# Kernel optimization log

Measured on AMD Instinct MI355X. Metric: run time of the kernel, lower is better.

## Reference

```python
import jax, jax.numpy as jnp
import numpy as np

N_NODES = 50000
N_EDGES = 800000
IN_DIM, HID_DIM, OUT_DIM = 128, 64, 64


def spmm(row, col, val, dense):
    # sparse [N,N] (COO) @ dense [N,D] -> [N,D]
    gathered = dense[col] * val[:, None]          # [E, D]
    return jax.ops.segment_sum(gathered, row, num_segments=N_NODES)


def setup_inputs() -> dict:
    key = jax.random.key(0)
    ks = jax.random.split(key, 8)
    stdv1 = 1.0 / np.sqrt(HID_DIM)
    stdv2 = 1.0 / np.sqrt(OUT_DIM)
    return {
        "x": jax.random.normal(ks[0], (N_NODES, IN_DIM), dtype=jnp.float32),
        "edge_row": jax.random.randint(ks[1], (N_EDGES,), 0, N_NODES, dtype=jnp.int32),
        "edge_col": jax.random.randint(ks[2], (N_EDGES,), 0, N_NODES, dtype=jnp.int32),
        "edge_val": jax.random.uniform(ks[3], (N_EDGES,), dtype=jnp.float32),
        "W1": jax.random.uniform(ks[4], (IN_DIM, HID_DIM), jnp.float32, -stdv1, stdv1),
        "b1": jax.random.uniform(ks[5], (HID_DIM,), jnp.float32, -stdv1, stdv1),
        "W2": jax.random.uniform(ks[6], (HID_DIM, OUT_DIM), jnp.float32, -stdv2, stdv2),
        "b2": jax.random.uniform(ks[7], (OUT_DIM,), jnp.float32, -stdv2, stdv2),
    }


def reference(x, edge_row, edge_col, edge_val, W1, b1, W2, b2):
    # layer 1: support = x @ W1; out = adj @ support + b1; relu
    h = jax.nn.relu(spmm(edge_row, edge_col, edge_val, x @ W1) + b1)
    # dropout: eval mode (training=False) -> identity
    # layer 2
    return spmm(edge_row, edge_col, edge_val, h @ W2) + b2
```

## Files before the change

### kernel.cpp

```cpp
#include <hip/hip_runtime.h>


#define N_NODES 50000
#define N_EDGES 800000
#define IN_DIM  128
#define HID_DIM 64
#define OUT_DIM 64

#define RB   256
#define NB   ((N_NODES + RB - 1) / RB)
#define EPB  4096
#define NBLK_E ((N_EDGES + EPB - 1) / EPB)
#define BCAP 5120
#define GEMM1_GRID ((N_NODES + 31) / 32)

typedef __attribute__((ext_vector_type(8))) short bf16x8;
typedef __attribute__((ext_vector_type(4))) float f32x4;

__device__ inline unsigned short f2bf(float x) {
    unsigned u = __float_as_uint(x);
    return (unsigned short)((u + 0x7FFFu + ((u >> 16) & 1u)) >> 16);
}
__device__ inline float bf2f(unsigned v) {
    return __uint_as_float(v << 16);
}

__global__ __launch_bounds__(256) void k_prep(
    const float* __restrict__ W1, unsigned short* __restrict__ Wt1,
    const float* __restrict__ W2, unsigned short* __restrict__ Wt2,
    int* __restrict__ bcur)
{
    int b = blockIdx.x, t = threadIdx.x;
    if (b < 32) {
        int e = b * 256 + t;
        int c = e / IN_DIM, k = e % IN_DIM;
        Wt1[c * IN_DIM + k] = f2bf(W1[k * HID_DIM + c]);
    } else if (b < 48) {
        int e2 = (b - 32) * 256 + t;
        int c = e2 / HID_DIM, k = e2 % HID_DIM;
        Wt2[c * HID_DIM + k] = f2bf(W2[k * OUT_DIM + c]);
    } else {
        if (t < NB) bcur[t] = 0;
    }
}

template <int K, bool IN_BF16>
__device__ __forceinline__ void gemm_body(
    unsigned short* __restrict__ Al, unsigned short* __restrict__ Bl,
    const void* __restrict__ Xv, const unsigned short* __restrict__ Wt,
    unsigned short* __restrict__ out, int bid, int t)
{
    int m0 = bid * 32;
    #pragma unroll
    for (int i = 0; i < K / 32; ++i) {
        int u4 = i * 256 + t;
        int col = (u4 * 8) / K, k = (u4 * 8) % K;
        uint4 w = ((const uint4*)Wt)[u4];
        int byte = (col * K + k) * 2;
        byte ^= ((col & 7) << 4);
        *(uint4*)((char*)Bl + byte) = w;
    }
    if (IN_BF16) {
        const unsigned short* X = (const unsigned short*)Xv;
        int row = t / (K / 8), k = (t % (K / 8)) * 8;
        int grow = m0 + row;
        uint4 v = make_uint4(0, 0, 0, 0);
        if (grow < N_NODES)
            v = *(const uint4*)(X + (size_t)grow * K + k);
        int byte = (row * K + k) * 2;
        byte ^= ((row & 7) << 4);
        *(uint4*)((char*)Al + byte) = v;
    } else {
        const float* X = (const float*)Xv;
        #pragma unroll
        for (int i = 0; i < K / 64; ++i) {
            int f8 = i * 256 + t;
            int row = (f8 * 8) / K, k = (f8 * 8) % K;
            int grow = m0 + row;
            float4 xa = make_float4(0.f, 0.f, 0.f, 0.f), xb = xa;
            if (grow < N_NODES) {
                const float4* src = (const float4*)(X + (size_t)grow * K + k);
                xa = src[0];
                xb = src[1];
            }
            uint4 v;
            v.x = (unsigned)f2bf(xa.x) | ((unsigned)f2bf(xa.y) << 16);
            v.y = (unsigned)f2bf(xa.z) | ((unsigned)f2bf(xa.w) << 16);
            v.z = (unsigned)f2bf(xb.x) | ((unsigned)f2bf(xb.y) << 16);
            v.w = (unsigned)f2bf(xb.z) | ((unsigned)f2bf(xb.w) << 16);
            int byte = (row * K + k) * 2;
            byte ^= ((row & 7) << 4);
            *(uint4*)((char*)Al + byte) = v;
        }
    }
    __syncthreads();

    int w = t >> 6, l = t & 63;
    int lr0 = (w & 1) * 16;
    int c0  = (w >> 1) * 32;
    int lrow = lr0 + (l & 15);
    int kb = (l >> 4) * 8;
    int col0 = c0 + (l & 15), col1 = col0 + 16;
    f32x4 acc0 = {0.f, 0.f, 0.f, 0.f}, acc1 = {0.f, 0.f, 0.f, 0.f};
    #pragma unroll
    for (int kc = 0; kc < K / 32; ++kc) {
        int ka = kc * 32 + kb;
        int ab = (lrow * K + ka) * 2;  ab ^= ((lrow & 7) << 4);
        int bb0 = (col0 * K + ka) * 2; bb0 ^= ((col0 & 7) << 4);
        int bb1 = (col1 * K + ka) * 2; bb1 ^= ((col1 & 7) << 4);
        bf16x8 a  = *(const bf16x8*)((const char*)Al + ab);
        bf16x8 b0 = *(const bf16x8*)((const char*)Bl + bb0);
        bf16x8 b1 = *(const bf16x8*)((const char*)Bl + bb1);
        acc0 = __builtin_amdgcn_mfma_f32_16x16x32_bf16(a, b0, acc0, 0, 0, 0);
        acc1 = __builtin_amdgcn_mfma_f32_16x16x32_bf16(a, b1, acc1, 0, 0, 0);
    }
    int grow0 = m0 + lr0 + (l >> 4) * 4;
    #pragma unroll
    for (int j = 0; j < 4; ++j) {
        int gr = grow0 + j;
        if (gr < N_NODES) {
            out[(size_t)gr * 64 + col0] = f2bf(acc0[j]);
            out[(size_t)gr * 64 + col1] = f2bf(acc1[j]);
        }
    }
}

__global__ __launch_bounds__(256) void k_mega1(
    const float* __restrict__ X, const unsigned short* __restrict__ Wt1,
    unsigned short* __restrict__ support,
    const int* __restrict__ erow, const int* __restrict__ ecol,
    const float* __restrict__ eval_, int* __restrict__ bcur,
    uint2* __restrict__ bucketed)
{
    __shared__ __align__(16) unsigned char smem[35392];
    int t = threadIdx.x;
    if (blockIdx.x < GEMM1_GRID) {
        gemm_body<IN_DIM, false>((unsigned short*)smem,
                                 (unsigned short*)(smem + 8192),
                                 X, Wt1, support, blockIdx.x, t);
        return;
    }
    uint2* sbuf  = (uint2*)smem;
    int*   lc    = (int*)(smem + 32768);
    int*   scr   = (int*)(smem + 33568);
    int*   lbase = (int*)(smem + 34592);
    int blk = blockIdx.x - GEMM1_GRID;
    if (t < NB) lc[t] = 0;
    __syncthreads();
    int base = blk * EPB;
    int ne_total = min(EPB, N_EDGES - base);
    int bkt[16], rnk[16];
    unsigned w0v[16], vv[16];
    #pragma unroll 4
    for (int i = 0; i < 16; ++i) {
        int e = base + i * 256 + t;
        bkt[i] = -1;
        if (e < N_EDGES) {
            unsigned r = (unsigned)erow[e];
            bkt[i] = (int)(r >> 8);
            w0v[i] = (unsigned)ecol[e] | ((r & 255u) << 16)
                     | ((unsigned)(r >> 8) << 24);
            vv[i] = __float_as_uint(eval_[e]);
            rnk[i] = atomicAdd(&lc[bkt[i]], 1);
        }
    }
    __syncthreads();
    int cnt = (t < NB) ? lc[t] : 0;
    scr[t] = cnt;
    __syncthreads();
    #pragma unroll
    for (int off = 1; off < 256; off <<= 1) {
        int add = (t >= off) ? scr[t - off] : 0;
        __syncthreads();
        scr[t] += add;
        __syncthreads();
    }
    int excl = scr[t] - cnt;
    __syncthreads();
    scr[t] = excl;
    if (t < NB) lbase[t] = cnt ? atomicAdd(&bcur[t], cnt) : 0;
    __syncthreads();
    #pragma unroll 4
    for (int i = 0; i < 16; ++i)
        if (bkt[i] >= 0)
            sbuf[scr[bkt[i]] + rnk[i]] = make_uint2(w0v[i], vv[i]);
    __syncthreads();
    #pragma unroll 4
    for (int i = 0; i < 16; ++i) {
        int idx = i * 256 + t;
        if (idx < ne_total) {
            uint2 p = sbuf[idx];
            int bk = (int)(p.x >> 24);
            bucketed[(size_t)bk * BCAP + lbase[bk] + (idx - scr[bk])] = p;
        }
    }
}

__global__ __launch_bounds__(256) void k_bfinal(
    const int* __restrict__ bcur, const uint2* __restrict__ bucketed,
    uint2* __restrict__ pairs, int2* __restrict__ offs2)
{
    __shared__ uint2 ebuf[BCAP];
    __shared__ int rcnt[256];
    __shared__ int rsc[256];
    int t = threadIdx.x, b = blockIdx.x;
    int ne = bcur[b];
    int base0 = b * BCAP;
    rcnt[t] = 0;
    __syncthreads();
    for (int i = t; i < ne; i += 256) {
        uint2 p = bucketed[(size_t)base0 + i];
        ebuf[i] = p;
        atomicAdd(&rcnt[(p.x >> 16) & 255], 1);
    }
    __syncthreads();
    int v = rcnt[t];
    rsc[t] = v;
    __syncthreads();
    #pragma unroll
    for (int off = 1; off < 256; off <<= 1) {
        int add = (t >= off) ? rsc[t - off] : 0;
        __syncthreads();
        rsc[t] += add;
        __syncthreads();
    }
    int start = base0 + rsc[t] - v;
    int gr = (b << 8) + t;
    if (gr < N_NODES) offs2[gr] = make_int2(start, start + v);
    rcnt[t] = start;
    __syncthreads();
    for (int i = t; i < ne; i += 256) {
        uint2 p = ebuf[i];
        int pos = atomicAdd(&rcnt[(p.x >> 16) & 255], 1);
        pairs[pos] = make_uint2(p.x & 0xFFFFu, p.y);
    }
}

template <bool APPLY_RELU, bool OUT_BF16>
__global__ __launch_bounds__(256) void k_gather(
    const int2* __restrict__ offs2, const uint2* __restrict__ pairs,
    const unsigned short* __restrict__ dense, const float* __restrict__ bias,
    void* __restrict__ outp)
{
    int t = threadIdx.x;
    int r = __builtin_amdgcn_readfirstlane(blockIdx.x * 4 + (t >> 6));
    int d = t & 63;
    int2 oe = offs2[r];
    int e0 = oe.x, e1 = oe.y;
    float a[8];
    a[0] = bias[d];
    #pragma unroll
    for (int i = 1; i < 8; ++i) a[i] = 0.f;
    int e = e0;
    for (; e + 8 <= e1; e += 8) {
        uint2 p[8];
        #pragma unroll
        for (int i = 0; i < 8; ++i) p[i] = pairs[e + i];
        unsigned v[8];
        #pragma unroll
        for (int i = 0; i < 8; ++i) v[i] = dense[(size_t)p[i].x * 64u + d];
        #pragma unroll
        for (int i = 0; i < 8; ++i)
            a[i] = fmaf(__uint_as_float(p[i].y), bf2f(v[i]), a[i]);
    }
    if (e + 4 <= e1) {
        uint2 p[4];
        #pragma unroll
        for (int i = 0; i < 4; ++i) p[i] = pairs[e + i];
        unsigned v[4];
        #pragma unroll
        for (int i = 0; i < 4; ++i) v[i] = dense[(size_t)p[i].x * 64u + d];
        #pragma unroll
        for (int i = 0; i < 4; ++i)
            a[i] = fmaf(__uint_as_float(p[i].y), bf2f(v[i]), a[i]);
        e += 4;
    }
    for (; e < e1; ++e) {
        uint2 p = pairs[e];
        a[0] = fmaf(__uint_as_float(p.y),
                    bf2f(dense[(size_t)p.x * 64u + d]), a[0]);
    }
    float acc = ((a[0] + a[1]) + (a[2] + a[3])) +
                ((a[4] + a[5]) + (a[6] + a[7]));
    if (APPLY_RELU) acc = fmaxf(acc, 0.f);
    if (OUT_BF16)
        ((unsigned short*)outp)[(size_t)r * 64 + d] = f2bf(acc);
    else
        ((float*)outp)[(size_t)r * 64 + d] = acc;
}

__global__ __launch_bounds__(256) void k_gemm2(
    const unsigned short* __restrict__ X, const unsigned short* __restrict__ Wt,
    unsigned short* __restrict__ out)
{
    __shared__ unsigned short Al[32 * HID_DIM];
    __shared__ unsigned short Bl[64 * HID_DIM];
    gemm_body<HID_DIM, true>(Al, Bl, X, Wt, out, blockIdx.x, threadIdx.x);
}

extern "C" void kernel_launch(void* const* d_in, const int* in_sizes, int n_in,
                              void* d_out, int out_size, void* d_ws, size_t ws_size,
                              hipStream_t stream)
{
    const float* x     = (const float*)d_in[0];
    const int*   erow  = (const int*)d_in[1];
    const int*   ecol  = (const int*)d_in[2];
    const float* eval_ = (const float*)d_in[3];
    const float* W1    = (const float*)d_in[4];
    const float* b1    = (const float*)d_in[5];
    const float* W2    = (const float*)d_in[6];
    const float* b2    = (const float*)d_in[7];
    float* out = (float*)d_out;

    uint2* pairs    = (uint2*)d_ws;
    uint2* bucketed = pairs + (size_t)NB * BCAP;
    unsigned short* support = (unsigned short*)(bucketed + (size_t)NB * BCAP);
    unsigned short* agg1 = support + (size_t)N_NODES * 64;
    unsigned short* Wt1 = agg1 + (size_t)N_NODES * 64;
    unsigned short* Wt2 = Wt1 + IN_DIM * HID_DIM;
    int*  bcur  = (int*)(Wt2 + HID_DIM * OUT_DIM);
    int2* offs2 = (int2*)(bcur + NB);

    const int row_grid = N_NODES / 4;

    k_prep<<<49, 256, 0, stream>>>(W1, Wt1, W2, Wt2, bcur);
    k_mega1<<<GEMM1_GRID + NBLK_E, 256, 0, stream>>>(
        x, Wt1, support, erow, ecol, eval_, bcur, bucketed);
    k_bfinal<<<NB, 256, 0, stream>>>(bcur, bucketed, pairs, offs2);
    k_gather<true, true><<<row_grid, 256, 0, stream>>>(
        offs2, pairs, support, b1, agg1);
    k_gemm2<<<GEMM1_GRID, 256, 0, stream>>>(agg1, Wt2, support);
    k_gather<false, false><<<row_grid, 256, 0, stream>>>(
        offs2, pairs, support, b2, out);
}
```

Before: 96.24 us.

## Fuse bucket finalization with first SpMM and halve row-bucket size

The bucket-finalize pass and the layer-1 gather are merged into one kernel, k_spmm1, with 512 threads per block. It sorts each bucket's edges into row order in shared memory and aggregates directly from shared column/value arrays, removing a launch and a global re-read of the sorted pairs. Row buckets shrink from 256 to 128 rows, so k_mega1 now needs a two-part scan because there are more than 256 buckets. The layer-2 gather now handles 8 rows per wave. The trade-off is far fewer blocks and waves, so latency hiding for the random support gathers may get worse.

New measurement: 122.0 us. +26.7%, slower.

```diff
diff --git a/kernel.cpp b/kernel.cpp
--- a/kernel.cpp
+++ b/kernel.cpp
@@ -7,11 +7,11 @@
 #define HID_DIM 64
 #define OUT_DIM 64
 
-#define RB   256
-#define NB   ((N_NODES + RB - 1) / RB)
+#define RB   128
+#define NBK  ((N_NODES + RB - 1) / RB)
 #define EPB  4096
 #define NBLK_E ((N_EDGES + EPB - 1) / EPB)
-#define BCAP 5120
+#define BCAP 2560
 #define GEMM1_GRID ((N_NODES + 31) / 32)
 
 typedef __attribute__((ext_vector_type(8))) short bf16x8;
@@ -40,7 +40,7 @@
         int c = e2 / HID_DIM, k = e2 % HID_DIM;
         Wt2[c * HID_DIM + k] = f2bf(W2[k * OUT_DIM + c]);
     } else {
-        if (t < NB) bcur[t] = 0;
+        for (int i = t; i < NBK; i += 256) bcur[i] = 0;
     }
 }
 
@@ -132,7 +132,7 @@
     const float* __restrict__ eval_, int* __restrict__ bcur,
     uint2* __restrict__ bucketed)
 {
-    __shared__ __align__(16) unsigned char smem[35392];
+    __shared__ __align__(16) unsigned char smem[38080];
     int t = threadIdx.x;
     if (blockIdx.x < GEMM1_GRID) {
         gemm_body<IN_DIM, false>((unsigned short*)smem,
@@ -142,10 +142,10 @@
     }
     uint2* sbuf  = (uint2*)smem;
     int*   lc    = (int*)(smem + 32768);
-    int*   scr   = (int*)(smem + 33568);
-    int*   lbase = (int*)(smem + 34592);
+    int*   scr   = (int*)(smem + 34432);
+    int*   lbase = (int*)(smem + 36480);
     int blk = blockIdx.x - GEMM1_GRID;
-    if (t < NB) lc[t] = 0;
+    for (int i = t; i < NBK; i += 256) lc[i] = 0;
     __syncthreads();
     int base = blk * EPB;
     int ne_total = min(EPB, N_EDGES - base);
@@ -157,16 +157,16 @@
         bkt[i] = -1;
         if (e < N_EDGES) {
             unsigned r = (unsigned)erow[e];
-            bkt[i] = (int)(r >> 8);
-            w0v[i] = (unsigned)ecol[e] | ((r & 255u) << 16)
-                     | ((unsigned)(r >> 8) << 24);
+            bkt[i] = (int)(r >> 7);
+            w0v[i] = (unsigned)ecol[e] | ((r & 127u) << 16)
+                     | ((r >> 7) << 23);
             vv[i] = __float_as_uint(eval_[e]);
             rnk[i] = atomicAdd(&lc[bkt[i]], 1);
         }
     }
     __syncthreads();
-    int cnt = (t < NB) ? lc[t] : 0;
-    scr[t] = cnt;
+    int c0 = lc[t], c1 = (t + 256 < NBK) ? lc[t + 256] : 0;
+    scr[t] = c0 + c1;
     __syncthreads();
     #pragma unroll
     for (int off = 1; off < 256; off <<= 1) {
@@ -175,118 +175,184 @@
         scr[t] += add;
         __syncthreads();
     }
-    int excl = scr[t] - cnt;
-    __syncthreads();
-    scr[t] = excl;
-    if (t < NB) lbase[t] = cnt ? atomicAdd(&bcur[t], cnt) : 0;
+    __syncthreads();
+    int pairExcl = scr[t] - (c0 + c1);
+    __shared__ int totFirst;
+    if (t == 255) totFirst = 0;
+    __syncthreads();
+    scr[t] = c0;
+    __syncthreads();
+    #pragma unroll
+    for (int off = 1; off < 256; off <<= 1) {
+        int add = (t >= off) ? scr[t - off] : 0;
+        __syncthreads();
+        scr[t] += add;
+        __syncthreads();
+    }
+    int exclA = scr[t] - c0;
+    int sumA  = scr[255];
+    __syncthreads();
+    scr[t] = c1;
+    __syncthreads();
+    #pragma unroll
+    for (int off = 1; off < 256; off <<= 1) {
+        int add = (t >= off) ? scr[t - off] : 0;
+        __syncthreads();
+        scr[t] += add;
+        __syncthreads();
+    }
+    int exclB = sumA + scr[t] - c1;
+    __syncthreads();
+    scr[t] = exclA;
+    if (t + 256 < NBK) lbase[t + 256] = 0;
+    __syncthreads();
+    if (t + 256 < NBK) scr[t + 256 - 256] = exclA;
+    __shared__ int scrHi[256];
+    scrHi[t] = exclB;
+    if (t < NBK && t < 256)
+        lbase[t] = c0 ? atomicAdd(&bcur[t], c0) : 0;
+    if (t + 256 < NBK)
+        lbase[t + 256] = c1 ? atomicAdd(&bcur[t + 256], c1) : 0;
     __syncthreads();
     #pragma unroll 4
     for (int i = 0; i < 16; ++i)
-        if (bkt[i] >= 0)
-            sbuf[scr[bkt[i]] + rnk[i]] = make_uint2(w0v[i], vv[i]);
+        if (bkt[i] >= 0) {
+            int st = (bkt[i] < 256) ? scr[bkt[i]] : scrHi[bkt[i] - 256];
+            sbuf[st + rnk[i]] = make_uint2(w0v[i], vv[i]);
+        }
     __syncthreads();
     #pragma unroll 4
     for (int i = 0; i < 16; ++i) {
         int idx = i * 256 + t;
         if (idx < ne_total) {
             uint2 p = sbuf[idx];
-            int bk = (int)(p.x >> 24);
-            bucketed[(size_t)bk * BCAP + lbase[bk] + (idx - scr[bk])] = p;
-        }
-    }
-}
-
-__global__ __launch_bounds__(256) void k_bfinal(
+            int bk = (int)(p.x >> 23);
+            int st = (bk < 256) ? scr[bk] : scrHi[bk - 256];
+            bucketed[(size_t)bk * BCAP + lbase[bk] + (idx - st)] = p;
+        }
+    }
+}
+
+__global__ __launch_bounds__(512) void k_spmm1(
     const int* __restrict__ bcur, const uint2* __restrict__ bucketed,
-    uint2* __restrict__ pairs, int2* __restrict__ offs2)
+    const unsigned short* __restrict__ support, const float* __restrict__ b1,
+    uint2* __restrict__ pairs, int2* __restrict__ offs2,
+    unsigned short* __restrict__ agg1)
 {
     __shared__ uint2 ebuf[BCAP];
-    __shared__ int rcnt[256];
-    __shared__ int rsc[256];
+    __shared__ unsigned short scol[BCAP];
+    __shared__ float sval[BCAP];
+    __shared__ int rcnt[RB], lstart[RB], rcur[RB];
     int t = threadIdx.x, b = blockIdx.x;
     int ne = bcur[b];
-    int base0 = b * BCAP;
-    rcnt[t] = 0;
-    __syncthreads();
-    for (int i = t; i < ne; i += 256) {
-        uint2 p = bucketed[(size_t)base0 + i];
+    size_t base0 = (size_t)b * BCAP;
+    if (t < RB) rcnt[t] = 0;
+    __syncthreads();
+    for (int i = t; i < ne; i += 512) {
+        uint2 p = bucketed[base0 + i];
         ebuf[i] = p;
-        atomicAdd(&rcnt[(p.x >> 16) & 255], 1);
-    }
-    __syncthreads();
-    int v = rcnt[t];
-    rsc[t] = v;
-    __syncthreads();
-    #pragma unroll
-    for (int off = 1; off < 256; off <<= 1) {
-        int add = (t >= off) ? rsc[t - off] : 0;
-        __syncthreads();
-        rsc[t] += add;
-        __syncthreads();
-    }
-    int start = base0 + rsc[t] - v;
-    int gr = (b << 8) + t;
-    if (gr < N_NODES) offs2[gr] = make_int2(start, start + v);
-    rcnt[t] = start;
-    __syncthreads();
-    for (int i = t; i < ne; i += 256) {
+        atomicAdd(&rcnt[(p.x >> 16) & 127], 1);
+    }
+    __syncthreads();
+    if (t < 64) {
+        int c0 = rcnt[2 * t], c1 = rcnt[2 * t + 1];
+        int s = c0 + c1, inc = s;
+        #pragma unroll
+        for (int off = 1; off < 64; off <<= 1) {
+            int o = __shfl_up(inc, off, 64);
+            if (t >= off) inc += o;
+        }
+        int excl = inc - s;
+        lstart[2 * t] = excl;
+        lstart[2 * t + 1] = excl + c0;
+        rcur[2 * t] = excl;
+        rcur[2 * t + 1] = excl + c0;
+        int gr = b * RB + 2 * t;
+        int gs = (int)base0 + excl;
+        if (gr < N_NODES) offs2[gr] = make_int2(gs, gs + c0);
+        if (gr + 1 < N_NODES) offs2[gr + 1] = make_int2(gs + c0, gs + c0 + c1);
+    }
+    __syncthreads();
+    for (int i = t; i < ne; i += 512) {
         uint2 p = ebuf[i];
-        int pos = atomicAdd(&rcnt[(p.x >> 16) & 255], 1);
-        pairs[pos] = make_uint2(p.x & 0xFFFFu, p.y);
-    }
-}
-
-template <bool APPLY_RELU, bool OUT_BF16>
-__global__ __launch_bounds__(256) void k_gather(
+        int row = (p.x >> 16) & 127;
+        int pos = atomicAdd(&rcur[row], 1);
+        scol[pos] = (unsigned short)(p.x & 0xFFFFu);
+        sval[pos] = __uint_as_float(p.y);
+        pairs[base0 + pos] = make_uint2(p.x & 0xFFFFu, p.y);
+    }
+    __syncthreads();
+    int w = t >> 6, d = t & 63;
+    #pragma unroll 1
+    for (int j = 0; j < 16; ++j) {
+        int rl = w * 16 + j;
+        int gr = b * RB + rl;
+        if (gr >= N_NODES) continue;
+        int e0 = lstart[rl], e1 = rcur[rl];
+        float a[8];
+        a[0] = b1[d];
+        #pragma unroll
+        for (int i = 1; i < 8; ++i) a[i] = 0.f;
+        int e = e0;
+        for (; e + 8 <= e1; e += 8) {
+            unsigned short c[8];
+            float vv[8];
+            #pragma unroll
+            for (int i = 0; i < 8; ++i) { c[i] = scol[e + i]; vv[i] = sval[e + i]; }
+            unsigned v[8];
+            #pragma unroll
+            for (int i = 0; i < 8; ++i) v[i] = support[(size_t)c[i] * 64u + d];
+            #pragma unroll
+            for (int i = 0; i < 8; ++i) a[i] = fmaf(vv[i], bf2f(v[i]), a[i]);
+        }
+        for (; e < e1; ++e)
+            a[0] = fmaf(sval[e], bf2f(support[(size_t)scol[e] * 64u + d]), a[0]);
+        float acc = ((a[0] + a[1]) + (a[2] + a[3])) +
+                    ((a[4] + a[5]) + (a[6] + a[7]));
+        acc = fmaxf(acc, 0.f);
+        agg1[(size_t)gr * 64 + d] = f2bf(acc);
+    }
+}
+
+__global__ __launch_bounds__(256) void k_gather2(
     const int2* __restrict__ offs2, const uint2* __restrict__ pairs,
     const unsigned short* __restrict__ dense, const float* __restrict__ bias,
-    void* __restrict__ outp)
+    float* __restrict__ outp)
 {
     int t = threadIdx.x;
-    int r = __builtin_amdgcn_readfirstlane(blockIdx.x * 4 + (t >> 6));
-    int d = t & 63;
-    int2 oe = offs2[r];
-    int e0 = oe.x, e1 = oe.y;
-    float a[8];
-    a[0] = bias[d];
-    #pragma unroll
-    for (int i = 1; i < 8; ++i) a[i] = 0.f;
-    int e = e0;
-    for (; e + 8 <= e1; e += 8) {
-        uint2 p[8];
+    int w = t >> 6, d = t & 63;
+    int rbase = __builtin_amdgcn_readfirstlane((blockIdx.x * 4 + w) * 8);
+    #pragma unroll 1
+    for (int j = 0; j < 8; ++j) {
+        int r = rbase + j;
+        if (r >= N_NODES) continue;
+        int2 oe = offs2[r];
+        int e0 = oe.x, e1 = oe.y;
+        float a[8];
+        a[0] = bias[d];
         #pragma unroll
-        for (int i = 0; i < 8; ++i) p[i] = pairs[e + i];
-        unsigned v[8];
-        #pragma unroll
-        for (int i = 0; i < 8; ++i) v[i] = dense[(size_t)p[i].x * 64u + d];
-        #pragma unroll
-        for (int i = 0; i < 8; ++i)
-            a[i] = fmaf(__uint_as_float(p[i].y), bf2f(v[i]), a[i]);
-    }
-    if (e + 4 <= e1) {
-        uint2 p[4];
-        #pragma unroll
-        for (int i = 0; i < 4; ++i) p[i] = pairs[e + i];
-        unsigned v[4];
-        #pragma unroll
-        for (int i = 0; i < 4; ++i) v[i] = dense[(size_t)p[i].x * 64u + d];
-        #pragma unroll
-        for (int i = 0; i < 4; ++i)
-            a[i] = fmaf(__uint_as_float(p[i].y), bf2f(v[i]), a[i]);
-        e += 4;
-    }
-    for (; e < e1; ++e) {
-        uint2 p = pairs[e];
-        a[0] = fmaf(__uint_as_float(p.y),
-                    bf2f(dense[(size_t)p.x * 64u + d]), a[0]);
-    }
-    float acc = ((a[0] + a[1]) + (a[2] + a[3])) +
-                ((a[4] + a[5]) + (a[6] + a[7]));
-    if (APPLY_RELU) acc = fmaxf(acc, 0.f);
-    if (OUT_BF16)
-        ((unsigned short*)outp)[(size_t)r * 64 + d] = f2bf(acc);
-    else
-        ((float*)outp)[(size_t)r * 64 + d] = acc;
+        for (int i = 1; i < 8; ++i) a[i] = 0.f;
+        int e = e0;
+        for (; e + 8 <= e1; e += 8) {
+            uint2 p[8];
+            #pragma unroll
+            for (int i = 0; i < 8; ++i) p[i] = pairs[e + i];
+            unsigned v[8];
+            #pragma unroll
+            for (int i = 0; i < 8; ++i) v[i] = dense[(size_t)p[i].x * 64u + d];
+            #pragma unroll
+            for (int i = 0; i < 8; ++i)
+                a[i] = fmaf(__uint_as_float(p[i].y), bf2f(v[i]), a[i]);
+        }
+        for (; e < e1; ++e) {
+            uint2 p = pairs[e];
+            a[0] = fmaf(__uint_as_float(p.y),
+                        bf2f(dense[(size_t)p.x * 64u + d]), a[0]);
+        }
+        float acc = ((a[0] + a[1]) + (a[2] + a[3])) +
+                    ((a[4] + a[5]) + (a[6] + a[7]));
+        outp[(size_t)r * 64 + d] = acc;
+    }
 }
 
 __global__ __launch_bounds__(256) void k_gemm2(
@@ -313,23 +379,20 @@
     float* out = (float*)d_out;
 
     uint2* pairs    = (uint2*)d_ws;
-    uint2* bucketed = pairs + (size_t)NB * BCAP;
-    unsigned short* support = (unsigned short*)(bucketed + (size_t)NB * BCAP);
+    uint2* bucketed = pairs + (size_t)NBK * BCAP;
+    unsigned short* support = (unsigned short*)(bucketed + (size_t)NBK * BCAP);
     unsigned short* agg1 = support + (size_t)N_NODES * 64;
     unsigned short* Wt1 = agg1 + (size_t)N_NODES * 64;
     unsigned short* Wt2 = Wt1 + IN_DIM * HID_DIM;
     int*  bcur  = (int*)(Wt2 + HID_DIM * OUT_DIM);
-    int2* offs2 = (int2*)(bcur + NB);
-
-    const int row_grid = N_NODES / 4;
+    int2* offs2 = (int2*)(bcur + NBK + 1);
 
     k_prep<<<49, 256, 0, stream>>>(W1, Wt1, W2, Wt2, bcur);
     k_mega1<<<GEMM1_GRID + NBLK_E, 256, 0, stream>>>(
         x, Wt1, support, erow, ecol, eval_, bcur, bucketed);
-    k_bfinal<<<NB, 256, 0, stream>>>(bcur, bucketed, pairs, offs2);
-    k_gather<true, true><<<row_grid, 256, 0, stream>>>(
-        offs2, pairs, support, b1, agg1);
+    k_spmm1<<<NBK, 512, 0, stream>>>(
+        bcur, bucketed, support, b1, pairs, offs2, agg1);
     k_gemm2<<<GEMM1_GRID, 256, 0, stream>>>(agg1, Wt2, support);
-    k_gather<false, false><<<row_grid, 256, 0, stream>>>(
+    k_gather2<<<(N_NODES + 31) / 32, 256, 0, stream>>>(
         offs2, pairs, support, b2, out);
 }
```

## Split fused GEMM1/bucket-scatter kernel into separate launches with smaller edge blocks

Applied to the files above, without the earlier changes.

Replaces the combined kernel that ran the first GEMM and the edge bucket scatter in one grid with separate scatter and GEMM1 kernels. The scatter now handles 1024 edges per block instead of 4096, cutting per-thread register arrays and shared memory so more blocks can be resident. This gives up the concurrency between the GEMM and the scatter, adds a launch, and raises global atomic traffic on the bucket counters.

Measured after the change: 98.86 us. 2.7% more time.

```diff
diff --git a/kernel.cpp b/kernel.cpp
--- a/kernel.cpp
+++ b/kernel.cpp
@@ -9,10 +9,10 @@
 
 #define RB   256
 #define NB   ((N_NODES + RB - 1) / RB)
-#define EPB  4096
+#define EPB  1024
 #define NBLK_E ((N_EDGES + EPB - 1) / EPB)
 #define BCAP 5120
-#define GEMM1_GRID ((N_NODES + 31) / 32)
+#define GEMM_GRID ((N_NODES + 31) / 32)
 
 typedef __attribute__((ext_vector_type(8))) short bf16x8;
 typedef __attribute__((ext_vector_type(4))) float f32x4;
@@ -41,6 +41,106 @@
         Wt2[c * HID_DIM + k] = f2bf(W2[k * OUT_DIM + c]);
     } else {
         if (t < NB) bcur[t] = 0;
+    }
+}
+
+__global__ __launch_bounds__(256) void k_bscatter(
+    const int* __restrict__ erow, const int* __restrict__ ecol,
+    const float* __restrict__ eval_, int* __restrict__ bcur,
+    uint2* __restrict__ bucketed)
+{
+    __shared__ uint2 sbuf[EPB];
+    __shared__ int lc[NB];
+    __shared__ int scr[256];
+    __shared__ int lbase[NB];
+    int t = threadIdx.x;
+    if (t < NB) lc[t] = 0;
+    __syncthreads();
+    int base = blockIdx.x * EPB;
+    int ne = min(EPB, N_EDGES - base);
+    int bkt[4], rnk[4];
+    unsigned w0v[4], vv[4];
+    #pragma unroll
+    for (int i = 0; i < 4; ++i) {
+        int e = base + i * 256 + t;
+        bkt[i] = -1;
+        if (e < N_EDGES) {
+            unsigned r = (unsigned)erow[e];
+            bkt[i] = (int)(r >> 8);
+            w0v[i] = (unsigned)ecol[e] | ((r & 255u) << 16) | ((r >> 8) << 24);
+            vv[i] = __float_as_uint(eval_[e]);
+            rnk[i] = atomicAdd(&lc[bkt[i]], 1);
+        }
+    }
+    __syncthreads();
+    int cnt = (t < NB) ? lc[t] : 0;
+    scr[t] = cnt;
+    __syncthreads();
+    #pragma unroll
+    for (int off = 1; off < 256; off <<= 1) {
+        int add = (t >= off) ? scr[t - off] : 0;
+        __syncthreads();
+        scr[t] += add;
+        __syncthreads();
+    }
+    int excl = scr[t] - cnt;
+    __syncthreads();
+    scr[t] = excl;
+    if (t < NB) lbase[t] = cnt ? atomicAdd(&bcur[t], cnt) : 0;
+    __syncthreads();
+    #pragma unroll
+    for (int i = 0; i < 4; ++i)
+        if (bkt[i] >= 0)
+            sbuf[scr[bkt[i]] + rnk[i]] = make_uint2(w0v[i], vv[i]);
+    __syncthreads();
+    #pragma unroll
+    for (int i = 0; i < 4; ++i) {
+        int idx = i * 256 + t;
+        if (idx < ne) {
+            uint2 p = sbuf[idx];
+            int bk = (int)(p.x >> 24);
+            bucketed[(size_t)bk * BCAP + lbase[bk] + (idx - scr[bk])] = p;
+        }
+    }
+}
+
+__global__ __launch_bounds__(256) void k_bfinal(
+    const int* __restrict__ bcur, const uint2* __restrict__ bucketed,
+    uint2* __restrict__ pairs, int2* __restrict__ offs2)
+{
+    __shared__ uint2 ebuf[BCAP];
+    __shared__ int rcnt[256];
+    __shared__ int rsc[256];
+    int t = threadIdx.x, b = blockIdx.x;
+    int ne = bcur[b];
+    int base0 = b * BCAP;
+    rcnt[t] = 0;
+    __syncthreads();
+    for (int i = t; i < ne; i += 256) {
+        uint2 p = bucketed[(size_t)base0 + i];
+        ebuf[i] = p;
+        atomicAdd(&rcnt[(p.x >> 16) & 255], 1);
+    }
+    __syncthreads();
+    int v = rcnt[t];
+    rsc[t] = v;
+    __syncthreads();
+    #pragma unroll
+    for (int off = 1; off < 256; off <<= 1) {
+        int add = (t >= off) ? rsc[t - off] : 0;
+        __syncthreads();
+        rsc[t] += add;
+        __syncthreads();
+    }
+    int start = base0 + rsc[t] - v;
+    int gr = (b << 8) + t;
+    if (gr < N_NODES) offs2[gr] = make_int2(start, start + v);
+    rcnt[t] = start;
+    __syncthreads();
+    for (int i = t; i < ne; i += 256) {
+        uint2 p = ebuf[i];
+        int pos = atomicAdd(&rcnt[(p.x >> 16) & 255], 1);
+        pairs[pos] = make_uint2(p.x & 0xFFFFu, p.y);
     }
 }
 
@@ -125,115 +225,22 @@
     }
 }
 
-__global__ __launch_bounds__(256) void k_mega1(
-    const float* __restrict__ X, const unsigned short* __restrict__ Wt1,
-    unsigned short* __restrict__ support,
-    const int* __restrict__ erow, const int* __restrict__ ecol,
-    const float* __restrict__ eval_, int* __restrict__ bcur,
-    uint2* __restrict__ bucketed)
-{
-    __shared__ __align__(16) unsigned char smem[35392];
-    int t = threadIdx.x;
-    if (blockIdx.x < GEMM1_GRID) {
-        gemm_body<IN_DIM, false>((unsigned short*)smem,
-                                 (unsigned short*)(smem + 8192),
-                                 X, Wt1, support, blockIdx.x, t);
-        return;
-    }
-    uint2* sbuf  = (uint2*)smem;
-    int*   lc    = (int*)(smem + 32768);
-    int*   scr   = (int*)(smem + 33568);
-    int*   lbase = (int*)(smem + 34592);
-    int blk = blockIdx.x - GEMM1_GRID;
-    if (t < NB) lc[t] = 0;
-    __syncthreads();
-    int base = blk * EPB;
-    int ne_total = min(EPB, N_EDGES - base);
-    int bkt[16], rnk[16];
-    unsigned w0v[16], vv[16];
-    #pragma unroll 4
-    for (int i = 0; i < 16; ++i) {
-        int e = base + i * 256 + t;
-        bkt[i] = -1;
-        if (e < N_EDGES) {
-            unsigned r = (unsigned)erow[e];
-            bkt[i] = (int)(r >> 8);
-            w0v[i] = (unsigned)ecol[e] | ((r & 255u) << 16)
-                     | ((unsigned)(r >> 8) << 24);
-            vv[i] = __float_as_uint(eval_[e]);
-            rnk[i] = atomicAdd(&lc[bkt[i]], 1);
-        }
-    }
-    __syncthreads();
-    int cnt = (t < NB) ? lc[t] : 0;
-    scr[t] = cnt;
-    __syncthreads();
-    #pragma unroll
-    for (int off = 1; off < 256; off <<= 1) {
-        int add = (t >= off) ? scr[t - off] : 0;
-        __syncthreads();
-        scr[t] += add;
-        __syncthreads();
-    }
-    int excl = scr[t] - cnt;
-    __syncthreads();
-    scr[t] = excl;
-    if (t < NB) lbase[t] = cnt ? atomicAdd(&bcur[t], cnt) : 0;
-    __syncthreads();
-    #pragma unroll 4
-    for (int i = 0; i < 16; ++i)
-        if (bkt[i] >= 0)
-            sbuf[scr[bkt[i]] + rnk[i]] = make_uint2(w0v[i], vv[i]);
-    __syncthreads();
-    #pragma unroll 4
-    for (int i = 0; i < 16; ++i) {
-        int idx = i * 256 + t;
-        if (idx < ne_total) {
-            uint2 p = sbuf[idx];
-            int bk = (int)(p.x >> 24);
-            bucketed[(size_t)bk * BCAP + lbase[bk] + (idx - scr[bk])] = p;
-        }
-    }
-}
-
-__global__ __launch_bounds__(256) void k_bfinal(
-    const int* __restrict__ bcur, const uint2* __restrict__ bucketed,
-    uint2* __restrict__ pairs, int2* __restrict__ offs2)
-{
-    __shared__ uint2 ebuf[BCAP];
-    __shared__ int rcnt[256];
-    __shared__ int rsc[256];
-    int t = threadIdx.x, b = blockIdx.x;
-    int ne = bcur[b];
-    int base0 = b * BCAP;
-    rcnt[t] = 0;
-    __syncthreads();
-    for (int i = t; i < ne; i += 256) {
-        uint2 p = bucketed[(size_t)base0 + i];
-        ebuf[i] = p;
-        atomicAdd(&rcnt[(p.x >> 16) & 255], 1);
-    }
-    __syncthreads();
-    int v = rcnt[t];
-    rsc[t] = v;
-    __syncthreads();
-    #pragma unroll
-    for (int off = 1; off < 256; off <<= 1) {
-        int add = (t >= off) ? rsc[t - off] : 0;
-        __syncthreads();
-        rsc[t] += add;
-        __syncthreads();
-    }
-    int start = base0 + rsc[t] - v;
-    int gr = (b << 8) + t;
-    if (gr < N_NODES) offs2[gr] = make_int2(start, start + v);
-    rcnt[t] = start;
-    __syncthreads();
-    for (int i = t; i < ne; i += 256) {
-        uint2 p = ebuf[i];
-        int pos = atomicAdd(&rcnt[(p.x >> 16) & 255], 1);
-        pairs[pos] = make_uint2(p.x & 0xFFFFu, p.y);
-    }
+__global__ __launch_bounds__(256) void k_gemm1(
+    const float* __restrict__ X, const unsigned short* __restrict__ Wt,
+    unsigned short* __restrict__ out)
+{
+    __shared__ unsigned short Al[32 * IN_DIM];
+    __shared__ unsigned short Bl[64 * IN_DIM];
+    gemm_body<IN_DIM, false>(Al, Bl, X, Wt, out, blockIdx.x, threadIdx.x);
+}
+
+__global__ __launch_bounds__(256) void k_gemm2(
+    const unsigned short* __restrict__ X, const unsigned short* __restrict__ Wt,
+    unsigned short* __restrict__ out)
+{
+    __shared__ unsigned short Al[32 * HID_DIM];
+    __shared__ unsigned short Bl[64 * HID_DIM];
+    gemm_body<HID_DIM, true>(Al, Bl, X, Wt, out, blockIdx.x, threadIdx.x);
 }
 
 template <bool APPLY_RELU, bool OUT_BF16>
@@ -287,15 +294,6 @@
         ((unsigned short*)outp)[(size_t)r * 64 + d] = f2bf(acc);
     else
         ((float*)outp)[(size_t)r * 64 + d] = acc;
-}
-
-__global__ __launch_bounds__(256) void k_gemm2(
-    const unsigned short* __restrict__ X, const unsigned short* __restrict__ Wt,
-    unsigned short* __restrict__ out)
-{
-    __shared__ unsigned short Al[32 * HID_DIM];
-    __shared__ unsigned short Bl[64 * HID_DIM];
-    gemm_body<HID_DIM, true>(Al, Bl, X, Wt, out, blockIdx.x, threadIdx.x);
 }
 
 extern "C" void kernel_launch(void* const* d_in, const int* in_sizes, int n_in,
@@ -324,12 +322,12 @@
     const int row_grid = N_NODES / 4;
 
     k_prep<<<49, 256, 0, stream>>>(W1, Wt1, W2, Wt2, bcur);
-    k_mega1<<<GEMM1_GRID + NBLK_E, 256, 0, stream>>>(
-        x, Wt1, support, erow, ecol, eval_, bcur, bucketed);
+    k_bscatter<<<NBLK_E, 256, 0, stream>>>(erow, ecol, eval_, bcur, bucketed);
     k_bfinal<<<NB, 256, 0, stream>>>(bcur, bucketed, pairs, offs2);
+    k_gemm1<<<GEMM_GRID, 256, 0, stream>>>(x, Wt1, support);
     k_gather<true, true><<<row_grid, 256, 0, stream>>>(
         offs2, pairs, support, b1, agg1);
-    k_gemm2<<<GEMM1_GRID, 256, 0, stream>>>(agg1, Wt2, support);
+    k_gemm2<<<GEMM_GRID, 256, 0, stream>>>(agg1, Wt2, support);
     k_gather<false, false><<<row_grid, 256, 0, stream>>>(
         offs2, pairs, support, b2, out);
 }
```
